# Kernel optimization log

Measured on AMD Instinct MI355X. Metric: run time of the kernel, lower is better.

The kernel has to match this reference:

```python
import jax, jax.numpy as jnp
import numpy as np

B, CIN, COUT, H, W = 2, 256, 256, 96, 96
K, PAD, G = 3, 1, 4           # kernel, padding, deformable_groups
KK = K * K
CG = CIN // G                 # channels per deformable group


def setup_inputs() -> dict:
    key = jax.random.key(0)
    k1, k2, k3, k4 = jax.random.split(key, 4)
    feature = jax.random.normal(k1, (B, CIN, H, W), jnp.float32)
    pred_shape = jax.random.normal(k2, (B, H * W, 4), jnp.float32)
    # init_weights: normal(std=0.01), no biases
    w_offset = jax.random.normal(k3, (G * KK * 2, 4, 1, 1), jnp.float32) * 0.01
    w_deform = jax.random.normal(k4, (COUT, CIN, K, K), jnp.float32) * 0.01
    return {"feature": feature, "pred_shape": pred_shape,
            "w_offset": w_offset, "w_deform": w_deform}


def reference(feature, pred_shape, w_offset, w_deform):
    # pred_shape: (B, H*W, 4) -> (B, 4, H, W); detached in the original
    ps = jnp.transpose(pred_shape, (0, 2, 1)).reshape(B, -1, H, W)
    ps = jax.lax.stop_gradient(ps)
    # 1x1 offset conv: (B, G*2*KK, H, W)
    offset = jnp.einsum('bchw,oc->bohw', ps, w_offset[:, :, 0, 0])
    # mmcv layout per group: [y_k0, x_k0, y_k1, x_k1, ...]
    off = offset.reshape(B, G, KK, 2, H, W)
    off_y, off_x = off[:, :, :, 0], off[:, :, :, 1]   # (B, G, KK, H, W)

    kk = jnp.arange(KK)
    ky = (kk // K).reshape(KK, 1, 1).astype(jnp.float32)
    kx = (kk % K).reshape(KK, 1, 1).astype(jnp.float32)
    yy = jnp.arange(H, dtype=jnp.float32).reshape(1, H, 1)
    xx = jnp.arange(W, dtype=jnp.float32).reshape(1, 1, W)
    # sampling positions (stride=1, dilation=1): (B, G, KK, H, W)
    py = (yy - PAD + ky)[None, None] + off_y
    px = (xx - PAD + kx)[None, None] + off_x

    img = feature.reshape(B, G, CG, H * W)

    def gather(yi, xi):
        # zero outside the image (matches DCN bilinear with zero padding)
        valid = ((yi >= 0) & (yi < H) & (xi >= 0) & (xi < W)).astype(feature.dtype)
        idx = jnp.clip(yi, 0, H - 1) * W + jnp.clip(xi, 0, W - 1)
        v = jnp.take_along_axis(img, idx.reshape(B, G, 1, KK * H * W), axis=3)
        return v.reshape(B, G, CG, KK, H, W) * valid[:, :, None]

    y0 = jnp.floor(py); x0 = jnp.floor(px)
    ly = py - y0; lx = px - x0
    y0i = y0.astype(jnp.int32); x0i = x0.astype(jnp.int32)

    val = ((1 - ly) * (1 - lx))[:, :, None] * gather(y0i, x0i) \
        + ((1 - ly) * lx)[:, :, None] * gather(y0i, x0i + 1) \
        + (ly * (1 - lx))[:, :, None] * gather(y0i + 1, x0i) \
        + (ly * lx)[:, :, None] * gather(y0i + 1, x0i + 1)

    sampled = val.reshape(B, CIN, KK, H, W)
    out = jnp.einsum('bckhw,ock->bohw', sampled, w_deform.reshape(COUT, CIN, KK))
    return jax.nn.relu(out)
```

## Files before the change

kernel.cpp:

```cpp
#include <hip/hip_runtime.h>
#include <hip/hip_bf16.h>
#include <stdint.h>

#define HH   96
#define WW   96
#define HW   9216
#define CIN  256
#define COUT 256
#define NB   2
#define NG   4
#define CG   64
#define KK   9
#define KTOT 2304
#define KB   288
#define TS   8
#define WIN  12
#define SCH  32

typedef __attribute__((ext_vector_type(8))) short short8;
typedef __attribute__((ext_vector_type(4))) float f32x4;
typedef __attribute__((ext_vector_type(4))) uint32_t u32x4;

__device__ __forceinline__ uint32_t pk2bf(float v0, float v1) {
    __hip_bfloat162 h = __float22bfloat162_rn(make_float2(v0, v1));
    uint32_t u;
    __builtin_memcpy(&u, &h, 4);
    return u;
}

__global__ __launch_bounds__(256) void prep_A(const float* __restrict__ wd,
                                              uint16_t* __restrict__ Ablk) {
    int t  = blockIdx.x * 256 + threadIdx.x;
    int kb = t % KB;
    int o  = t / KB;
    int kkA = kb >> 5;
    int c0A = (kb & 31) * 8;
    const float* src = wd + (size_t)o * KTOT + c0A * KK + kkA;
    float a[8];
#pragma unroll
    for (int e = 0; e < 8; ++e) a[e] = src[e * KK];
    int my = o >> 7, ol = o & 127;
    uint16_t* dst = Ablk + (((size_t)my * KB + kb) * 128 + ol) * 8;
    u32x4 v;
    v.x = pk2bf(a[0], a[1]);
    v.y = pk2bf(a[2], a[3]);
    v.z = pk2bf(a[4], a[5]);
    v.w = pk2bf(a[6], a[7]);
    *(u32x4*)dst = v;
}

__global__ __launch_bounds__(256) void sampler(const float* __restrict__ feature,
                                               const float* __restrict__ pred,
                                               const float* __restrict__ woff,
                                               uint16_t* __restrict__ S) {
    __shared__ float ft[SCH * WIN * WIN];

    int tid = threadIdx.x;
    int cb = blockIdx.y, b = blockIdx.z;
    int ch0 = cb * SCH;
    int g = ch0 >> 6;
    int ty = blockIdx.x / (WW / TS), tx = blockIdx.x % (WW / TS);
    int r0 = ty * TS, c0 = tx * TS;
    int rlo = min(max(r0 - 2, 0), HH - WIN);
    int clo = min(max(c0 - 2, 0), WW - WIN);

    const float* fg = feature + ((size_t)(b * CIN + ch0)) * HW;
    for (int e = tid; e < SCH * WIN * WIN; e += 256) {
        int ch = e / (WIN * WIN);
        int re = e - ch * (WIN * WIN);
        int rr = re / WIN, cc = re - rr * WIN;
        ft[e] = fg[(size_t)ch * HW + (rlo + rr) * WW + clo + cc];
    }
    __syncthreads();

    int lane = tid & 63, wv = tid >> 6;
    int lr = lane >> 3, lc = lane & 7;
    int hy = r0 + lr, hx = c0 + lc;
    int p = hy * WW + hx;
    float4 ps4 = *(const float4*)(pred + ((size_t)b * HW + p) * 4);

    const float* ftw = ft + (wv * 8) * (WIN * WIN);
    const float* fgw = fg + (size_t)(wv * 8) * HW;
    int kb_base = cb * 4 + wv;

#pragma unroll
    for (int kk = 0; kk < KK; ++kk) {
        const float* wy = woff + (g * KK + kk) * 8;
        float offy = ps4.x * wy[0] + ps4.y * wy[1] + ps4.z * wy[2] + ps4.w * wy[3];
        float offx = ps4.x * wy[4] + ps4.y * wy[5] + ps4.z * wy[6] + ps4.w * wy[7];
        float py = (float)(hy - 1 + kk / 3) + offy;
        float px = (float)(hx - 1 + kk % 3) + offx;
        float fy = floorf(py), fx = floorf(px);
        int y0 = (int)fy, x0 = (int)fx;
        float ly = py - fy, lx = px - fx;
        int r = min(max(y0, 0), HH - 2);
        int q = min(max(x0, 0), WW - 2);
        float wyA = (y0 == r) ? (1.f - ly) : ((y0 == -1) ? ly : 0.f);
        float wyB = (y0 == r) ? ly : ((y0 == HH - 1) ? (1.f - ly) : 0.f);
        float wxA = (x0 == q) ? (1.f - lx) : ((x0 == -1) ? lx : 0.f);
        float wxB = (x0 == q) ? lx : ((x0 == WW - 1) ? (1.f - lx) : 0.f);
        float c00 = wyA * wxA, c01 = wyA * wxB;
        float c10 = wyB * wxA, c11 = wyB * wxB;

        bool fast = (r >= rlo) & (r <= rlo + WIN - 2) &
                    (q >= clo) & (q <= clo + WIN - 2);

        uint16_t* Sp = S + (((size_t)b * KB + (kk * 32 + kb_base)) * HW + p) * 8;
        uint32_t pk[4];

        if (fast) {
            int base = (r - rlo) * WIN + (q - clo);
#pragma unroll
            for (int ep = 0; ep < 4; ++ep) {
                const float* f0 = ftw + (2 * ep) * (WIN * WIN) + base;
                const float* f1 = f0 + (WIN * WIN);
                float v0 = c00 * f0[0] + c01 * f0[1] + c10 * f0[WIN] + c11 * f0[WIN + 1];
                float v1 = c00 * f1[0] + c01 * f1[1] + c10 * f1[WIN] + c11 * f1[WIN + 1];
                pk[ep] = pk2bf(v0, v1);
            }
        } else {
            size_t gb = (size_t)r * WW + q;
#pragma unroll
            for (int ep = 0; ep < 4; ++ep) {
                const float* f0 = fgw + (size_t)(2 * ep) * HW + gb;
                const float* f1 = f0 + HW;
                float v0 = c00 * f0[0] + c01 * f0[1] + c10 * f0[WW] + c11 * f0[WW + 1];
                float v1 = c00 * f1[0] + c01 * f1[1] + c10 * f1[WW] + c11 * f1[WW + 1];
                pk[ep] = pk2bf(v0, v1);
            }
        }
        u32x4 vv = {pk[0], pk[1], pk[2], pk[3]};
        *(u32x4*)(Sp) = vv;
    }
}

__global__ __launch_bounds__(256) void gemm_kernel(const uint16_t* __restrict__ S,
                                                   const uint16_t* __restrict__ Ablk,
                                                   float* __restrict__ out) {
    __shared__ uint16_t sA[4][4 * 128 * 8];
    __shared__ uint16_t sB[4][4 * 64 * 8];

    int tid = threadIdx.x;
    int lane = tid & 63, wv = tid >> 6;
    int wr = wv >> 1, wc = wv & 1;
    int col0 = blockIdx.x * 64;
    int my   = blockIdx.y;
    int b    = blockIdx.z;

    const uint16_t* Ag = Ablk + (size_t)my * KB * 128 * 8;
    const uint16_t* Bg = S    + (size_t)b  * KB * HW  * 8;

    f32x4 acc[4][2];
#pragma unroll
    for (int m = 0; m < 4; ++m)
#pragma unroll
        for (int n = 0; n < 2; ++n) acc[m][n] = (f32x4){0.f, 0.f, 0.f, 0.f};

    int kc = lane >> 4, il = lane & 15;
    const int NT = KTOT / 32;

    auto STAGE = [&](int t, int buf) {
        const uint16_t* ga = Ag + ((size_t)(t * 4 + wv) * 128) * 8;
        uint16_t* la = &sA[buf][wv * 128 * 8];
#pragma unroll
        for (int h = 0; h < 2; ++h) {
            __builtin_amdgcn_global_load_lds(
                (const __attribute__((address_space(1))) uint32_t*)(ga + (h * 64 + lane) * 8),
                (__attribute__((address_space(3))) uint32_t*)(la + h * 64 * 8),
                16, 0, 0);
        }
        const uint16_t* gb = Bg + ((size_t)(t * 4 + wv) * HW + col0) * 8;
        uint16_t* lb = &sB[buf][wv * 64 * 8];
        __builtin_amdgcn_global_load_lds(
            (const __attribute__((address_space(1))) uint32_t*)(gb + lane * 8),
            (__attribute__((address_space(3))) uint32_t*)(lb),
            16, 0, 0);
    };

    STAGE(0, 0);
    STAGE(1, 1);
    STAGE(2, 2);
    STAGE(3, 3);

    for (int t = 0; t < NT; ++t) {
        int cur = t & 3;
        if (t < NT - 3) {
            asm volatile("s_waitcnt vmcnt(9)\n\ts_barrier" ::: "memory");
        } else if (t == NT - 3) {
            asm volatile("s_waitcnt vmcnt(6)\n\ts_barrier" ::: "memory");
        } else if (t == NT - 2) {
            asm volatile("s_waitcnt vmcnt(3)\n\ts_barrier" ::: "memory");
        } else {
            asm volatile("s_waitcnt vmcnt(0)\n\ts_barrier" ::: "memory");
        }
        __builtin_amdgcn_sched_barrier(0);

        short8 af[4], bf[2];
#pragma unroll
        for (int m = 0; m < 4; ++m)
            af[m] = *(const short8*)(&sA[cur][((kc * 128) + (wr * 64 + m * 16 + il)) * 8]);
#pragma unroll
        for (int n = 0; n < 2; ++n)
            bf[n] = *(const short8*)(&sB[cur][((kc * 64) + (wc * 32 + n * 16 + il)) * 8]);

#pragma unroll
        for (int m = 0; m < 4; ++m)
#pragma unroll
            for (int n = 0; n < 2; ++n)
                acc[m][n] = __builtin_amdgcn_mfma_f32_16x16x32_bf16(af[m], bf[n], acc[m][n], 0, 0, 0);

        asm volatile("s_waitcnt lgkmcnt(0)\n\ts_barrier" ::: "memory");
        __builtin_amdgcn_sched_barrier(0);
        if (t + 4 < NT) STAGE(t + 4, cur);
    }

    int r4 = (lane >> 4) * 4;
    size_t obase = ((size_t)b * COUT + my * 128 + wr * 64) * HW + col0 + wc * 32;
#pragma unroll
    for (int m = 0; m < 4; ++m)
#pragma unroll
        for (int n = 0; n < 2; ++n)
#pragma unroll
            for (int r = 0; r < 4; ++r) {
                float v = acc[m][n][r];
                v = v > 0.f ? v : 0.f;
                out[obase + (size_t)(m * 16 + r4 + r) * HW + n * 16 + il] = v;
            }
}

extern "C" void kernel_launch(void* const* d_in, const int* in_sizes, int n_in,
                              void* d_out, int out_size, void* d_ws, size_t ws_size,
                              hipStream_t stream) {
    (void)in_sizes; (void)n_in; (void)out_size; (void)ws_size;
    const float* feature = (const float*)d_in[0];
    const float* pred    = (const float*)d_in[1];
    const float* woff    = (const float*)d_in[2];
    const float* wdef    = (const float*)d_in[3];
    float* out = (float*)d_out;

    const size_t S_BYTES = (size_t)NB * KB * HW * 8 * 2;
    uint16_t* S    = (uint16_t*)d_ws;
    uint16_t* Ablk = (uint16_t*)((char*)d_ws + S_BYTES);

    hipLaunchKernelGGL(prep_A, dim3(288), dim3(256), 0, stream, wdef, Ablk);
    hipLaunchKernelGGL(sampler, dim3((HH / TS) * (WW / TS), CIN / SCH, NB), dim3(256), 0, stream,
                       feature, pred, woff, S);
    hipLaunchKernelGGL(gemm_kernel, dim3(HW / 64, 2, NB), dim3(256), 0, stream,
                       S, Ablk, out);
}
```

Measured before the change: 86.28 us.

## Shrink GEMM tile to 64x64 with 64-deep K steps and double buffering

The GEMM output tile per block shrinks from 128x64 to 64x64, giving twice as many blocks (4 row-blocks instead of 2) to raise occupancy and parallelism. Each K step now covers 64 instead of 32, and the 4-deep LDS ring becomes a 2-deep double buffer. The A weight layout in prep_A changes to a plain [kb][o] order so any 64-row slice can be loaded. B tiles are now fetched twice as often across blocks, which costs more global/L2 traffic and lowers MFMA reuse per LDS load.

```diff
diff --git a/kernel.cpp b/kernel.cpp
--- a/kernel.cpp
+++ b/kernel.cpp
@@ -39,8 +39,7 @@
     float a[8];
 #pragma unroll
     for (int e = 0; e < 8; ++e) a[e] = src[e * KK];
-    int my = o >> 7, ol = o & 127;
-    uint16_t* dst = Ablk + (((size_t)my * KB + kb) * 128 + ol) * 8;
+    uint16_t* dst = Ablk + ((size_t)kb * 256 + o) * 8;
     u32x4 v;
     v.x = pk2bf(a[0], a[1]);
     v.y = pk2bf(a[2], a[3]);
@@ -137,87 +136,87 @@
 __global__ __launch_bounds__(256) void gemm_kernel(const uint16_t* __restrict__ S,
                                                    const uint16_t* __restrict__ Ablk,
                                                    float* __restrict__ out) {
-    __shared__ uint16_t sA[4][4 * 128 * 8];
-    __shared__ uint16_t sB[4][4 * 64 * 8];
+    __shared__ uint16_t sA[2][8 * 64 * 8];
+    __shared__ uint16_t sB[2][8 * 64 * 8];
 
     int tid = threadIdx.x;
     int lane = tid & 63, wv = tid >> 6;
     int wr = wv >> 1, wc = wv & 1;
     int col0 = blockIdx.x * 64;
-    int my   = blockIdx.y;
+    int o0   = blockIdx.y * 64;
     int b    = blockIdx.z;
 
-    const uint16_t* Ag = Ablk + (size_t)my * KB * 128 * 8;
-    const uint16_t* Bg = S    + (size_t)b  * KB * HW  * 8;
-
-    f32x4 acc[4][2];
-#pragma unroll
-    for (int m = 0; m < 4; ++m)
+    const uint16_t* Bg = S + (size_t)b * KB * HW * 8;
+
+    f32x4 acc[2][2];
+#pragma unroll
+    for (int m = 0; m < 2; ++m)
 #pragma unroll
         for (int n = 0; n < 2; ++n) acc[m][n] = (f32x4){0.f, 0.f, 0.f, 0.f};
 
     int kc = lane >> 4, il = lane & 15;
-    const int NT = KTOT / 32;
+    const int NT = KTOT / 64;
 
     auto STAGE = [&](int t, int buf) {
-        const uint16_t* ga = Ag + ((size_t)(t * 4 + wv) * 128) * 8;
-        uint16_t* la = &sA[buf][wv * 128 * 8];
-#pragma unroll
-        for (int h = 0; h < 2; ++h) {
+#pragma unroll
+        for (int j = 0; j < 2; ++j) {
+            int kb = t * 8 + wv * 2 + j;
+            int lc_ = wv * 2 + j;
             __builtin_amdgcn_global_load_lds(
-                (const __attribute__((address_space(1))) uint32_t*)(ga + (h * 64 + lane) * 8),
-                (__attribute__((address_space(3))) uint32_t*)(la + h * 64 * 8),
+                (const __attribute__((address_space(1))) uint32_t*)
+                    (Ablk + ((size_t)kb * 256 + o0 + lane) * 8),
+                (__attribute__((address_space(3))) uint32_t*)
+                    (&sA[buf][(lc_ * 64 + lane) * 8]),
                 16, 0, 0);
-        }
-        const uint16_t* gb = Bg + ((size_t)(t * 4 + wv) * HW + col0) * 8;
-        uint16_t* lb = &sB[buf][wv * 64 * 8];
-        __builtin_amdgcn_global_load_lds(
-            (const __attribute__((address_space(1))) uint32_t*)(gb + lane * 8),
-            (__attribute__((address_space(3))) uint32_t*)(lb),
-            16, 0, 0);
+            __builtin_amdgcn_global_load_lds(
+                (const __attribute__((address_space(1))) uint32_t*)
+                    (Bg + ((size_t)kb * HW + col0 + lane) * 8),
+                (__attribute__((address_space(3))) uint32_t*)
+                    (&sB[buf][(lc_ * 64 + lane) * 8]),
+                16, 0, 0);
+        }
     };
 
     STAGE(0, 0);
     STAGE(1, 1);
-    STAGE(2, 2);
-    STAGE(3, 3);
 
     for (int t = 0; t < NT; ++t) {
-        int cur = t & 3;
-        if (t < NT - 3) {
-            asm volatile("s_waitcnt vmcnt(9)\n\ts_barrier" ::: "memory");
-        } else if (t == NT - 3) {
-            asm volatile("s_waitcnt vmcnt(6)\n\ts_barrier" ::: "memory");
-        } else if (t == NT - 2) {
-            asm volatile("s_waitcnt vmcnt(3)\n\ts_barrier" ::: "memory");
+        int cur = t & 1;
+        if (t < NT - 1) {
+            asm volatile("s_waitcnt vmcnt(4)\n\ts_barrier" ::: "memory");
         } else {
             asm volatile("s_waitcnt vmcnt(0)\n\ts_barrier" ::: "memory");
         }
         __builtin_amdgcn_sched_barrier(0);
 
-        short8 af[4], bf[2];
-#pragma unroll
-        for (int m = 0; m < 4; ++m)
-            af[m] = *(const short8*)(&sA[cur][((kc * 128) + (wr * 64 + m * 16 + il)) * 8]);
-#pragma unroll
-        for (int n = 0; n < 2; ++n)
-            bf[n] = *(const short8*)(&sB[cur][((kc * 64) + (wc * 32 + n * 16 + il)) * 8]);
-
-#pragma unroll
-        for (int m = 0; m < 4; ++m)
+        short8 af[2][2], bf[2][2];
+#pragma unroll
+        for (int h = 0; h < 2; ++h) {
+#pragma unroll
+            for (int m = 0; m < 2; ++m)
+                af[h][m] = *(const short8*)(&sA[cur][((h * 4 + kc) * 64 + wr * 32 + m * 16 + il) * 8]);
 #pragma unroll
             for (int n = 0; n < 2; ++n)
-                acc[m][n] = __builtin_amdgcn_mfma_f32_16x16x32_bf16(af[m], bf[n], acc[m][n], 0, 0, 0);
+                bf[h][n] = *(const short8*)(&sB[cur][((h * 4 + kc) * 64 + wc * 32 + n * 16 + il) * 8]);
+        }
+
+#pragma unroll
+        for (int h = 0; h < 2; ++h)
+#pragma unroll
+            for (int m = 0; m < 2; ++m)
+#pragma unroll
+                for (int n = 0; n < 2; ++n)
+                    acc[m][n] = __builtin_amdgcn_mfma_f32_16x16x32_bf16(af[h][m], bf[h][n], acc[m][n], 0, 0, 0);
 
         asm volatile("s_waitcnt lgkmcnt(0)\n\ts_barrier" ::: "memory");
         __builtin_amdgcn_sched_barrier(0);
-        if (t + 4 < NT) STAGE(t + 4, cur);
+        if (t + 2 < NT) STAGE(t + 2, cur);
     }
 
     int r4 = (lane >> 4) * 4;
-    size_t obase = ((size_t)b * COUT + my * 128 + wr * 64) * HW + col0 + wc * 32;
-#pragma unroll
-    for (int m = 0; m < 4; ++m)
+    size_t obase = ((size_t)b * COUT + o0 + wr * 32) * HW + col0 + wc * 32;
+#pragma unroll
+    for (int m = 0; m < 2; ++m)
 #pragma unroll
         for (int n = 0; n < 2; ++n)
 #pragma unroll
@@ -245,6 +244,6 @@
     hipLaunchKernelGGL(prep_A, dim3(288), dim3(256), 0, stream, wdef, Ablk);
     hipLaunchKernelGGL(sampler, dim3((HH / TS) * (WW / TS), CIN / SCH, NB), dim3(256), 0, stream,
                        feature, pred, woff, S);
-    hipLaunchKernelGGL(gemm_kernel, dim3(HW / 64, 2, NB), dim3(256), 0, stream,
+    hipLaunchKernelGGL(gemm_kernel, dim3(HW / 64, COUT / 64, NB), dim3(256), 0, stream,
                        S, Ablk, out);
 }
```

Measured after the change: 93.72 us. 8.6% more time.
